# Performance work log

Hardware: AMD Instinct MI355X
Metric: run time of the kernel (lower is better)

The kernel has to match this reference:

```python
import jax, jax.numpy as jnp
import numpy as np

NEG_INF = -9e15
ALPHA = 0.2  # leaky_relu slope


def gat_layer(h, adj, e_feat, W, We, a_s, a_d, a_e, h_res):
    """Dense multi-head GAT layer with edge features.
    h: [B,N,Fin], adj: [B,N,N] (0/1), e_feat: [B,N,N,Ein]
    W: [H,Fin,Fout], We: [H,Ein,Eout], a_s/a_d: [H,Fout], a_e: [H,Eout]
    Returns head-averaged (x_prime [B,N,Fout], e_prime [B,N,N,Eout]).
    """
    Wh = jnp.einsum('bnf,hfo->bhno', h, W)            # [B,H,N,Fout]
    Me = jnp.einsum('bnmf,hfe->bhnme', e_feat, We)    # [B,H,N,N,Eout]
    s_src = jnp.einsum('bhno,ho->bhn', Wh, a_s)
    s_dst = jnp.einsum('bhno,ho->bhn', Wh, a_d)
    s_edge = jnp.einsum('bhnme,he->bhnm', Me, a_e)
    scores = jax.nn.leaky_relu(s_src[:, :, :, None] + s_dst[:, :, None, :] + s_edge, ALPHA)
    scores = jnp.where(adj[:, None, :, :] > 0, scores, NEG_INF)
    att = jax.nn.softmax(scores, axis=-1)             # [B,H,N,N]
    h_prime = jnp.einsum('bhnm,bhmo->bhno', att, Wh)
    h_prime = jax.nn.elu(h_prime) + h_res[:, None]    # concat=True -> elu; residual add
    e_prime = att[..., None] * Me                      # attention-modulated edge features
    return h_prime.mean(axis=1), e_prime.mean(axis=1)


def setup_inputs() -> dict:
    key = jax.random.key(0)
    ks = jax.random.split(key, 16)
    B, N, F, E, H = 2, 256, 768, 7, 2
    nhid, ehid = 768, 768 // 2
    sc = lambda fan: 1.0 / np.sqrt(fan)
    return {
        'x': jax.random.normal(ks[0], (B, N, F), jnp.float32),
        'adj': jax.random.randint(ks[1], (B, N, N), 0, 2, jnp.int32),
        'e': jax.random.uniform(ks[2], (B, N, N, E), jnp.float32),
        'W1': jax.random.normal(ks[3], (H, F, nhid), jnp.float32) * sc(F),
        'We1': jax.random.normal(ks[4], (H, E, ehid), jnp.float32) * sc(E),
        'a1s': jax.random.normal(ks[5], (H, nhid), jnp.float32) * sc(nhid),
        'a1d': jax.random.normal(ks[6], (H, nhid), jnp.float32) * sc(nhid),
        'a1e': jax.random.normal(ks[7], (H, ehid), jnp.float32) * sc(ehid),
        'W2': jax.random.normal(ks[8], (H, nhid, nhid), jnp.float32) * sc(nhid),
        'We2': jax.random.normal(ks[9], (H, ehid, ehid), jnp.float32) * sc(ehid),
        'a2s': jax.random.normal(ks[10], (H, nhid), jnp.float32) * sc(nhid),
        'a2d': jax.random.normal(ks[11], (H, nhid), jnp.float32) * sc(nhid),
        'a2e': jax.random.normal(ks[12], (H, ehid), jnp.float32) * sc(ehid),
    }


def reference(x, adj, e, W1, We1, a1s, a1d, a1e, W2, We2, a2s, a2d, a2e):
    # dropout layers are identity in eval mode
    x1, e1 = gat_layer(x, adj, e, W1, We1, a1s, a1d, a1e, x)
    x2, e2 = gat_layer(x1, adj, e1, W2, We2, a2s, a2d, a2e, x)
    return x2, e2
```

## Files before the change

### kernel.cpp

```cpp
#include <hip/hip_runtime.h>
#include <hip/hip_bf16.h>
#include <cstddef>


typedef __attribute__((ext_vector_type(8))) short bf16x8;
typedef __attribute__((ext_vector_type(4))) short bf16x4;
typedef __attribute__((ext_vector_type(4))) float f32x4;
typedef unsigned short us;

#define DEVINL static __device__ __forceinline__

DEVINL us f2bf(float f) {
    union { float f; unsigned u; } v; v.f = f;
    return (us)((v.u + 0x7FFFu + ((v.u >> 16) & 1u)) >> 16);
}
DEVINL float bf2f(us b) {
    union { unsigned u; float f; } v; v.u = ((unsigned)b) << 16; return v.f;
}
DEVINL float wredmax(float v) {
#pragma unroll
    for (int s = 32; s; s >>= 1) v = fmaxf(v, __shfl_xor(v, s));
    return v;
}
DEVINL float wredsum(float v) {
#pragma unroll
    for (int s = 32; s; s >>= 1) v += __shfl_xor(v, s);
    return v;
}

DEVINL void transpose_body(const float* __restrict__ W, us* __restrict__ WT, int bb) {
    __shared__ us tile[64][65];
    const int ft = (bb % 12) * 64, ot = ((bb / 12) % 12) * 64, h = bb / 144;
    const int t = threadIdx.x;
    const float* Wh = W + (size_t)h * 768 * 768;
    us* WTh = WT + (size_t)h * 768 * 768;
#pragma unroll
    for (int i = 0; i < 16; i++) {
        int idx = t + i * 256, r = idx >> 6, c = idx & 63;
        tile[c][r] = f2bf(Wh[(ft + r) * 768 + ot + c]);
    }
    __syncthreads();
#pragma unroll
    for (int i = 0; i < 16; i++) {
        int idx = t + i * 256, r = idx >> 6, c = idx & 63;
        WTh[(ot + r) * 768 + ft + c] = tile[r][c];
    }
}

DEVINL void cvt_body(const float* __restrict__ in, us* __restrict__ out, int blk) {
    int i = (blk * 256 + threadIdx.x) * 4;
    float4 v = *(const float4*)&in[i];
    us pk[4] = {f2bf(v.x), f2bf(v.y), f2bf(v.z), f2bf(v.w)};
    *(bf16x4*)&out[i] = *(bf16x4*)pk;
}

DEVINL void pre_body(const float* __restrict__ W1, const float* __restrict__ W2,
                     const float* __restrict__ We1, const float* __restrict__ We2,
                     const float* __restrict__ a1s, const float* __restrict__ a1d,
                     const float* __restrict__ a1e, const float* __restrict__ a2s,
                     const float* __restrict__ a2d,
                     float* __restrict__ q, float* __restrict__ u1,
                     float* __restrict__ Mcat, int blk) {
    const int g = blk * 32 + (threadIdx.x >> 3);
    const int lane = threadIdx.x & 7;
    float acc = 0.0f;
    if (g < 6144) {
        int vec = g / 1536, rem = g % 1536, h = rem / 768, f = rem % 768;
        const float* W = (vec < 2) ? W1 : W2;
        const float* a = (vec == 0) ? a1s : (vec == 1) ? a1d : (vec == 2) ? a2s : a2d;
        const float* wr = W + (size_t)(h * 768 + f) * 768;
        const float* ar = a + h * 768;
        for (int o = lane; o < 768; o += 8) acc += wr[o] * ar[o];
        for (int s = 4; s; s >>= 1) acc += __shfl_down(acc, s, 8);
        if (lane == 0) q[g] = acc;
    } else if (g < 6160) {
        int g2 = g - 6144, h = g2 >> 3, k = g2 & 7;
        if (k < 7) {
            const float* wr = We1 + (h * 7 + k) * 384;
            const float* ar = a1e + h * 384;
            for (int o = lane; o < 384; o += 8) acc += wr[o] * ar[o];
        }
        for (int s = 4; s; s >>= 1) acc += __shfl_down(acc, s, 8);
        if (lane == 0) u1[g2] = acc;
    } else if (g < 18448) {
        int g3 = g - 6160, rk = g3 / 384, tc = g3 % 384;
        int hh = rk >> 3, kk = rk & 7, h1 = hh >> 1, h2 = hh & 1;
        if (kk < 7) {
            const float* wr = We1 + (h1 * 7 + kk) * 384;
            const float* w2c = We2 + (size_t)h2 * 384 * 384 + tc;
            for (int o = lane; o < 384; o += 8) acc += wr[o] * w2c[o * 384];
            acc *= 0.25f;
        }
        for (int s = 4; s; s >>= 1) acc += __shfl_down(acc, s, 8);
        if (lane == 0) Mcat[g3] = acc;
    }
}

DEVINL void wcalc_body(const float* __restrict__ Mcat, const float* __restrict__ a2e,
                       float* __restrict__ w) {
    const int t = threadIdx.x, g = t >> 3, lane = t & 7;
    int hh = g >> 3, k = g & 7, h2 = hh & 1;
    float acc = 0.0f;
    if (k < 7)
        for (int o = lane; o < 384; o += 8) acc += Mcat[(hh * 8 + k) * 384 + o] * a2e[h2 * 384 + o];
    for (int s = 4; s; s >>= 1) acc += __shfl_down(acc, s, 8);
    if (lane == 0) w[g] = 2.0f * acc;
}

DEVINL void bfrag_body(const float* __restrict__ Mcat, us* __restrict__ Bfrag, int ct) {
    const int l = threadIdx.x;
    if (l < 64) {
        us pk[8];
#pragma unroll
        for (int j = 0; j < 8; j++)
            pk[j] = f2bf(Mcat[((l >> 4) * 8 + j) * 384 + ct * 16 + (l & 15)]);
        *(bf16x8*)&Bfrag[(ct * 64 + l) * 8] = *(bf16x8*)pk;
    }
}

DEVINL void sdots_body(const float* __restrict__ x, const float* __restrict__ qs,
                       const float* __restrict__ qd, float* __restrict__ out_s,
                       float* __restrict__ out_d, int n, int b) {
    const int t = threadIdx.x, wv = t >> 6;
    const float* xr = x + (size_t)(b * 256 + n) * 768;
    float a0 = 0, a1 = 0, a2 = 0, a3 = 0;
#pragma unroll
    for (int i = 0; i < 3; i++) {
        int k = i * 256 + t;
        float xv = xr[k];
        a0 += xv * qs[k];
        a1 += xv * qs[768 + k];
        a2 += xv * qd[k];
        a3 += xv * qd[768 + k];
    }
    a0 = wredsum(a0); a1 = wredsum(a1); a2 = wredsum(a2); a3 = wredsum(a3);
    __shared__ float part[4][4];
    if ((t & 63) == 0) { part[wv][0] = a0; part[wv][1] = a1; part[wv][2] = a2; part[wv][3] = a3; }
    __syncthreads();
    if (t == 0) {
        float r0 = 0, r1 = 0, r2 = 0, r3 = 0;
#pragma unroll
        for (int i = 0; i < 4; i++) { r0 += part[i][0]; r1 += part[i][1]; r2 += part[i][2]; r3 += part[i][3]; }
        out_s[(b * 2 + 0) * 256 + n] = r0;
        out_s[(b * 2 + 1) * 256 + n] = r1;
        out_d[(b * 2 + 0) * 256 + n] = r2;
        out_d[(b * 2 + 1) * 256 + n] = r3;
    }
}

DEVINL void att_finish(float sc, us* __restrict__ attb, size_t outbase) {
    const int m = threadIdx.x, wv = m >> 6;
    __shared__ float sm[4], ssu[4];
    float wm_ = wredmax(sc);
    if ((m & 63) == 0) sm[wv] = wm_;
    __syncthreads();
    float mx = fmaxf(fmaxf(sm[0], sm[1]), fmaxf(sm[2], sm[3]));
    float ex = __expf(sc - mx);
    float ws = wredsum(ex);
    if ((m & 63) == 0) ssu[wv] = ws;
    __syncthreads();
    float inv = 1.0f / (ssu[0] + ssu[1] + ssu[2] + ssu[3]);
    attb[outbase + m] = f2bf(ex * inv);
}

DEVINL void att1_body(const float* __restrict__ e, const int* __restrict__ adj,
                      const float* __restrict__ s_s, const float* __restrict__ s_d,
                      const float* __restrict__ u1, us* __restrict__ attb,
                      int n, int h, int b) {
    const int m = threadIdx.x;
    float ss = s_s[(b * 2 + h) * 256 + n];
    float sd = s_d[(b * 2 + h) * 256 + m];
    const float* ep = e + ((size_t)(b * 256 + n) * 256 + m) * 7;
    float se = 0.0f;
#pragma unroll
    for (int k = 0; k < 7; k++) se += ep[k] * u1[h * 8 + k];
    float sc = ss + sd + se;
    sc = sc > 0.0f ? sc : 0.2f * sc;
    sc = adj[(size_t)(b * 256 + n) * 256 + m] > 0 ? sc : -9e15f;
    att_finish(sc, attb, ((size_t)(b * 2 + h) * 256 + n) * 256);
}

DEVINL void att2_body(const float* __restrict__ e, const int* __restrict__ adj,
                      const float* __restrict__ s_s, const float* __restrict__ s_d,
                      const float* __restrict__ w, const us* __restrict__ att1b,
                      us* __restrict__ attb, int n, int h, int b) {
    const int m = threadIdx.x;
    float ss = s_s[(b * 2 + h) * 256 + n];
    float sd = s_d[(b * 2 + h) * 256 + m];
    const float* ep = e + ((size_t)(b * 256 + n) * 256 + m) * 7;
    float se = 0.0f;
#pragma unroll
    for (int h1 = 0; h1 < 2; h1++) {
        float ew = 0.0f;
#pragma unroll
        for (int k = 0; k < 7; k++) ew += ep[k] * w[(h1 * 2 + h) * 8 + k];
        float a1 = bf2f(att1b[((size_t)(b * 2 + h1) * 256 + n) * 256 + m]);
        se += a1 * ew;
    }
    float sc = ss + sd + se;
    sc = sc > 0.0f ? sc : 0.2f * sc;
    sc = adj[(size_t)(b * 256 + n) * 256 + m] > 0 ? sc : -9e15f;
    att_finish(sc, attb, ((size_t)(b * 2 + h) * 256 + n) * 256);
}

DEVINL void gemm_xw_body(const us* __restrict__ A, const us* __restrict__ BT,
                         us* __restrict__ WhT, int mt, int ot, int h) {
    const int t = threadIdx.x, wv = t >> 6, l = t & 63;
    const int wm = wv >> 1, wn = wv & 1, lr = l & 15, lk = l >> 4;
    __shared__ us As[64][40];
    __shared__ us Bs[64][40];
    const int arow = t >> 2, acol = (t & 3) * 8;
    const us* Bh = BT + (size_t)h * 768 * 768;
    f32x4 acc[2][2];
#pragma unroll
    for (int i = 0; i < 2; i++)
#pragma unroll
        for (int j = 0; j < 2; j++) acc[i][j] = (f32x4){0, 0, 0, 0};
    for (int k0 = 0; k0 < 768; k0 += 32) {
        __syncthreads();
        *(bf16x8*)&As[arow][acol] = *(const bf16x8*)&A[(size_t)(mt * 64 + arow) * 768 + k0 + acol];
        *(bf16x8*)&Bs[arow][acol] = *(const bf16x8*)&Bh[(size_t)(ot * 64 + arow) * 768 + k0 + acol];
        __syncthreads();
        bf16x8 af[2], bfv[2];
#pragma unroll
        for (int i = 0; i < 2; i++) af[i] = *(const bf16x8*)&As[wm * 32 + i * 16 + lr][lk * 8];
#pragma unroll
        for (int j = 0; j < 2; j++) bfv[j] = *(const bf16x8*)&Bs[wn * 32 + j * 16 + lr][lk * 8];
#pragma unroll
        for (int i = 0; i < 2; i++)
#pragma unroll
            for (int j = 0; j < 2; j++)
                acc[i][j] = __builtin_amdgcn_mfma_f32_16x16x32_bf16(af[i], bfv[j], acc[i][j], 0, 0, 0);
    }
#pragma unroll
    for (int i = 0; i < 2; i++)
#pragma unroll
        for (int j = 0; j < 2; j++) {
            int n0 = mt * 64 + wm * 32 + i * 16 + lk * 4;
            int og = ot * 64 + wn * 32 + j * 16 + lr;
            int b = n0 >> 8, n = n0 & 255;
            us pk[4];
#pragma unroll
            for (int r = 0; r < 4; r++) pk[r] = f2bf(acc[i][j][r]);
            *(bf16x4*)&WhT[((size_t)(b * 2 + h) * 768 + og) * 256 + n] = *(bf16x4*)pk;
        }
}

DEVINL void gemm_att_body(const us* __restrict__ attb, const us* __restrict__ WhT,
                          const float* __restrict__ resid, float* __restrict__ xout,
                          us* __restrict__ xbout, int mt, int ot, int b) {
    const int t = threadIdx.x, wv = t >> 6, l = t & 63;
    const int wm = wv >> 1, wn = wv & 1, lr = l & 15, lk = l >> 4;
    __shared__ us As2[64][40];
    __shared__ us Bs2[64][40];
    const int arow = t >> 2, acol = (t & 3) * 8;
    float res[2][2][4] = {};
    for (int h = 0; h < 2; h++) {
        const us* Ah = attb + (size_t)(b * 2 + h) * 256 * 256;
        const us* Bh = WhT + (size_t)(b * 2 + h) * 768 * 256;
        f32x4 acc[2][2];
#pragma unroll
        for (int i = 0; i < 2; i++)
#pragma unroll
            for (int j = 0; j < 2; j++) acc[i][j] = (f32x4){0, 0, 0, 0};
        for (int k0 = 0; k0 < 256; k0 += 32) {
            __syncthreads();
            *(bf16x8*)&As2[arow][acol] = *(const bf16x8*)&Ah[(size_t)(mt * 64 + arow) * 256 + k0 + acol];
            *(bf16x8*)&Bs2[arow][acol] = *(const bf16x8*)&Bh[(size_t)(ot * 64 + arow) * 256 + k0 + acol];
            __syncthreads();
            bf16x8 af[2], bfv[2];
#pragma unroll
            for (int i = 0; i < 2; i++) af[i] = *(const bf16x8*)&As2[wm * 32 + i * 16 + lr][lk * 8];
#pragma unroll
            for (int j = 0; j < 2; j++) bfv[j] = *(const bf16x8*)&Bs2[wn * 32 + j * 16 + lr][lk * 8];
#pragma unroll
            for (int i = 0; i < 2; i++)
#pragma unroll
                for (int j = 0; j < 2; j++)
                    acc[i][j] = __builtin_amdgcn_mfma_f32_16x16x32_bf16(af[i], bfv[j], acc[i][j], 0, 0, 0);
        }
#pragma unroll
        for (int i = 0; i < 2; i++)
#pragma unroll
            for (int j = 0; j < 2; j++)
#pragma unroll
                for (int r = 0; r < 4; r++) {
                    float v = acc[i][j][r];
                    res[i][j][r] += (v > 0.0f ? v : (expf(v) - 1.0f));
                }
        __syncthreads();
    }
#pragma unroll
    for (int i = 0; i < 2; i++)
#pragma unroll
        for (int j = 0; j < 2; j++) {
            int n0 = mt * 64 + wm * 32 + i * 16 + lk * 4;
            int og = ot * 64 + wn * 32 + j * 16 + lr;
#pragma unroll
            for (int r = 0; r < 4; r++) {
                size_t idx = (size_t)(b * 256 + n0 + r) * 768 + og;
                float v = 0.5f * res[i][j][r] + resid[idx];
                xout[idx] = v;
                if (xbout) xbout[idx] = f2bf(v);
            }
        }
}

DEVINL void e2_body(const float* __restrict__ e, const us* __restrict__ att1b,
                    const us* __restrict__ att2b, const us* __restrict__ Bfrag,
                    float* __restrict__ e2out, int eb, int cg) {
    __shared__ us bl[8 * 64 * 8];
    const int t = threadIdx.x;
    for (int idx = t; idx < 512; idx += 256)
        *(bf16x8*)&bl[idx * 8] = *(const bf16x8*)&Bfrag[(size_t)(cg * 512 + idx) * 8];
    __syncthreads();
    const int wv = t >> 6, l = t & 63, le = l & 15, lq = l >> 4;
    const int h1 = lq >> 1, h2 = lq & 1;
    bf16x8 bfr[8];
#pragma unroll
    for (int i = 0; i < 8; i++) bfr[i] = *(const bf16x8*)&bl[(i * 64 + l) * 8];
    const f32x4 zero = {0, 0, 0, 0};
    for (int g = 0; g < 4; g++) {
        const int ebase = eb * 256 + g * 64 + wv * 16;
        const int eidx = ebase + le;
        const int b = eidx >> 16, nm = eidx & 65535;
        float a1 = bf2f(att1b[(size_t)(b * 2 + h1) * 65536 + nm]);
        float a2 = bf2f(att2b[(size_t)(b * 2 + h2) * 65536 + nm]);
        float c = a1 * a2;
        const float* ep = e + (size_t)eidx * 7;
        us av[8];
#pragma unroll
        for (int j = 0; j < 7; j++) av[j] = f2bf(c * ep[j]);
        av[7] = 0;
        bf16x8 gfr = *(bf16x8*)av;
#pragma unroll
        for (int i = 0; i < 8; i++) {
            f32x4 accv = __builtin_amdgcn_mfma_f32_16x16x32_bf16(bfr[i], gfr, zero, 0, 0, 0);
            int o0 = cg * 128 + i * 16 + lq * 4;
            *(f32x4*)&e2out[(size_t)eidx * 384 + o0] = accv;
        }
    }
}

__global__ __launch_bounds__(256) void stage1(
    const float* W1, const float* W2, const float* We1, const float* We2,
    const float* a1s, const float* a1d, const float* a1e,
    const float* a2s, const float* a2d,
    const float* x, us* W1T, us* W2T, us* xb,
    float* q, float* u1, float* Mcat) {
    int b = blockIdx.x;
    if (b < 288)       transpose_body(W1, W1T, b);
    else if (b < 576)  transpose_body(W2, W2T, b - 288);
    else if (b < 960)  cvt_body(x, xb, b - 576);
    else               pre_body(W1, W2, We1, We2, a1s, a1d, a1e, a2s, a2d, q, u1, Mcat, b - 960);
}

__global__ __launch_bounds__(256) void stage2(
    const float* Mcat, const float* a2e, float* wbuf, us* Bfrag,
    const float* x, const float* qs, const float* qd, float* s1s, float* s1d) {
    int b = blockIdx.x;
    if (b < 1)        wcalc_body(Mcat, a2e, wbuf);
    else if (b < 25)  bfrag_body(Mcat, Bfrag, b - 1);
    else { int i = b - 25; sdots_body(x, qs, qd, s1s, s1d, i & 255, i >> 8); }
}

__global__ __launch_bounds__(256) void stage3(
    const float* e, const int* adj, const float* s1s, const float* s1d,
    const float* u1, us* att1b, const us* xb, const us* W1T, us* WhT1) {
    int b = blockIdx.x;
    if (b < 1024) att1_body(e, adj, s1s, s1d, u1, att1b, b & 255, (b >> 8) & 1, b >> 9);
    else { int g = b - 1024; gemm_xw_body(xb, W1T, WhT1, g & 7, (g >> 3) % 12, g / 96); }
}

__global__ __launch_bounds__(256) void stage4(
    const us* att1b, const us* WhT1, const float* x, float* x1, us* xb1) {
    int b = blockIdx.x;
    gemm_att_body(att1b, WhT1, x, x1, xb1, b & 3, (b >> 2) % 12, b / 48);
}

__global__ __launch_bounds__(256) void stage5(
    const float* x1, const float* qs, const float* qd, float* s2s, float* s2d,
    const us* xb1, const us* W2T, us* WhT2) {
    int b = blockIdx.x;
    if (b < 512) sdots_body(x1, qs, qd, s2s, s2d, b & 255, b >> 8);
    else { int g = b - 512; gemm_xw_body(xb1, W2T, WhT2, g & 7, (g >> 3) % 12, g / 96); }
}

__global__ __launch_bounds__(256) void stage6(
    const float* e, const int* adj, const float* s2s, const float* s2d,
    const float* wbuf, const us* att1b, us* att2b) {
    int b = blockIdx.x;
    att2_body(e, adj, s2s, s2d, wbuf, att1b, att2b, b & 255, (b >> 8) & 1, b >> 9);
}

__global__ __launch_bounds__(256) void stage7(
    const us* att2b, const us* WhT2, const float* x, float* x2out,
    const float* e, const us* att1b, const us* Bfrag, float* e2out) {
    int b = blockIdx.x;
    if (b < 96) gemm_att_body(att2b, WhT2, x, x2out, (us*)nullptr, b & 3, (b >> 2) % 12, b / 48);
    else { int idx = b - 96; e2_body(e, att1b, att2b, Bfrag, e2out, idx / 3, idx % 3); }
}

__global__ __launch_bounds__(256) void stage8(
    const float* e, const us* att1b, const us* att2b, const us* Bfrag, float* e2out) {
    int b = blockIdx.x;
    e2_body(e, att1b, att2b, Bfrag, e2out, 508 + b / 3, b % 3);
}

extern "C" void kernel_launch(void* const* d_in, const int* in_sizes, int n_in,
                              void* d_out, int out_size, void* d_ws, size_t ws_size,
                              hipStream_t stream) {
    const float* x   = (const float*)d_in[0];
    const int*   adj = (const int*)d_in[1];
    const float* e   = (const float*)d_in[2];
    const float* W1  = (const float*)d_in[3];
    const float* We1 = (const float*)d_in[4];
    const float* a1s = (const float*)d_in[5];
    const float* a1d = (const float*)d_in[6];
    const float* a1e = (const float*)d_in[7];
    const float* W2  = (const float*)d_in[8];
    const float* We2 = (const float*)d_in[9];
    const float* a2s = (const float*)d_in[10];
    const float* a2d = (const float*)d_in[11];
    const float* a2e = (const float*)d_in[12];

    float* out   = (float*)d_out;
    float* x2out = out;
    float* e2out = out + 393216;

    char* ws = (char*)d_ws;
    float* q     = (float*)(ws + 0);
    float* u1    = (float*)(ws + 24576);
    float* wbuf  = (float*)(ws + 24640);
    float* Mcat  = (float*)(ws + 24832);
    us*    Bfrag = (us*)(ws + 73984);
    float* s1s   = (float*)(ws + 98560);
    float* s1d   = (float*)(ws + 102656);
    float* s2s   = (float*)(ws + 106752);
    float* s2d   = (float*)(ws + 110848);
    us*    att1b = (us*)(ws + 114944);
    us*    att2b = (us*)(ws + 639232);

    char* sc = (char*)e2out;
    us*    W1T  = (us*)(sc + 0);
    us*    W2T  = (us*)(sc + 2359296);
    us*    xb   = (us*)(sc + 4718592);
    us*    xb1  = (us*)(sc + 5505024);
    us*    WhT1 = (us*)(sc + 6291456);
    float* x1   = (float*)(sc + 7864320);
    us*    WhT2 = (us*)(e2out + 49938432);

    stage1<<<1537, 256, 0, stream>>>(W1, W2, We1, We2, a1s, a1d, a1e, a2s, a2d,
                                     x, W1T, W2T, xb, q, u1, Mcat);
    stage2<<<537, 256, 0, stream>>>(Mcat, a2e, wbuf, Bfrag, x, q + 0, q + 1536, s1s, s1d);
    stage3<<<1216, 256, 0, stream>>>(e, adj, s1s, s1d, u1, att1b, xb, W1T, WhT1);
    stage4<<<96, 256, 0, stream>>>(att1b, WhT1, x, x1, xb1);
    stage5<<<704, 256, 0, stream>>>(x1, q + 3072, q + 4608, s2s, s2d, xb1, W2T, WhT2);
    stage6<<<1024, 256, 0, stream>>>(e, adj, s2s, s2d, wbuf, att1b, att2b);
    stage7<<<1620, 256, 0, stream>>>(att2b, WhT2, x, x2out, e, att1b, Bfrag, e2out);
    stage8<<<12, 256, 0, stream>>>(e, att1b, att2b, Bfrag, e2out);
}
```

Baseline: 118.3 us.

## Fuse both heads per attention row, retile att GEMM, row-wise e2, move scratch to workspace

Attention-score kernels now process both heads per block, staging the edge-feature row in shared memory once instead of reading it per head. The att@Wh GEMM is retiled to 32-row tiles to double block count, and the e2 output kernel now handles one full (b,n) row per block with all three column groups, removing the tail stage8 launch. Transpose and convert bodies use wider vector stores, scratch buffers move from the output region into the workspace, and stage1 block order is reshuffled. Larger shared-memory use in e2row may reduce occupancy.

```diff
diff --git a/kernel.cpp b/kernel.cpp
--- a/kernel.cpp
+++ b/kernel.cpp
@@ -41,17 +41,22 @@
     }
     __syncthreads();
 #pragma unroll
-    for (int i = 0; i < 16; i++) {
-        int idx = t + i * 256, r = idx >> 6, c = idx & 63;
-        WTh[(ot + r) * 768 + ft + c] = tile[r][c];
+    for (int i = 0; i < 2; i++) {
+        int idx = t + i * 256, r = idx >> 3, c0 = (idx & 7) * 8;
+        us pk[8];
+#pragma unroll
+        for (int j = 0; j < 8; j++) pk[j] = tile[r][c0 + j];
+        *(bf16x8*)&WTh[(ot + r) * 768 + ft + c0] = *(bf16x8*)pk;
     }
 }
 
 DEVINL void cvt_body(const float* __restrict__ in, us* __restrict__ out, int blk) {
-    int i = (blk * 256 + threadIdx.x) * 4;
-    float4 v = *(const float4*)&in[i];
-    us pk[4] = {f2bf(v.x), f2bf(v.y), f2bf(v.z), f2bf(v.w)};
-    *(bf16x4*)&out[i] = *(bf16x4*)pk;
+    int i = (blk * 256 + threadIdx.x) * 8;
+    float4 v0 = *(const float4*)&in[i];
+    float4 v1 = *(const float4*)&in[i + 4];
+    us pk[8] = {f2bf(v0.x), f2bf(v0.y), f2bf(v0.z), f2bf(v0.w),
+                f2bf(v1.x), f2bf(v1.y), f2bf(v1.z), f2bf(v1.w)};
+    *(bf16x8*)&out[i] = *(bf16x8*)pk;
 }
 
 DEVINL void pre_body(const float* __restrict__ W1, const float* __restrict__ W2,
@@ -148,59 +153,88 @@
     }
 }
 
-DEVINL void att_finish(float sc, us* __restrict__ attb, size_t outbase) {
-    const int m = threadIdx.x, wv = m >> 6;
-    __shared__ float sm[4], ssu[4];
-    float wm_ = wredmax(sc);
-    if ((m & 63) == 0) sm[wv] = wm_;
-    __syncthreads();
-    float mx = fmaxf(fmaxf(sm[0], sm[1]), fmaxf(sm[2], sm[3]));
-    float ex = __expf(sc - mx);
-    float ws = wredsum(ex);
-    if ((m & 63) == 0) ssu[wv] = ws;
-    __syncthreads();
-    float inv = 1.0f / (ssu[0] + ssu[1] + ssu[2] + ssu[3]);
-    attb[outbase + m] = f2bf(ex * inv);
+DEVINL void att_finish2(float sc0, float sc1, us* __restrict__ attb,
+                        size_t base0, size_t base1) {
+    const int t = threadIdx.x, wv = t >> 6;
+    __shared__ float smax[2][4], ssum[2][4];
+    float w0 = wredmax(sc0), w1 = wredmax(sc1);
+    if ((t & 63) == 0) { smax[0][wv] = w0; smax[1][wv] = w1; }
+    __syncthreads();
+    float mx0 = fmaxf(fmaxf(smax[0][0], smax[0][1]), fmaxf(smax[0][2], smax[0][3]));
+    float mx1 = fmaxf(fmaxf(smax[1][0], smax[1][1]), fmaxf(smax[1][2], smax[1][3]));
+    float ex0 = __expf(sc0 - mx0), ex1 = __expf(sc1 - mx1);
+    float su0 = wredsum(ex0), su1 = wredsum(ex1);
+    if ((t & 63) == 0) { ssum[0][wv] = su0; ssum[1][wv] = su1; }
+    __syncthreads();
+    float i0 = 1.0f / (ssum[0][0] + ssum[0][1] + ssum[0][2] + ssum[0][3]);
+    float i1 = 1.0f / (ssum[1][0] + ssum[1][1] + ssum[1][2] + ssum[1][3]);
+    attb[base0 + t] = f2bf(ex0 * i0);
+    attb[base1 + t] = f2bf(ex1 * i1);
 }
 
 DEVINL void att1_body(const float* __restrict__ e, const int* __restrict__ adj,
                       const float* __restrict__ s_s, const float* __restrict__ s_d,
                       const float* __restrict__ u1, us* __restrict__ attb,
-                      int n, int h, int b) {
-    const int m = threadIdx.x;
-    float ss = s_s[(b * 2 + h) * 256 + n];
-    float sd = s_d[(b * 2 + h) * 256 + m];
-    const float* ep = e + ((size_t)(b * 256 + n) * 256 + m) * 7;
-    float se = 0.0f;
-#pragma unroll
-    for (int k = 0; k < 7; k++) se += ep[k] * u1[h * 8 + k];
-    float sc = ss + sd + se;
-    sc = sc > 0.0f ? sc : 0.2f * sc;
-    sc = adj[(size_t)(b * 256 + n) * 256 + m] > 0 ? sc : -9e15f;
-    att_finish(sc, attb, ((size_t)(b * 2 + h) * 256 + n) * 256);
+                      int n, int bb) {
+    __shared__ float eL[1792];
+    const int t = threadIdx.x;
+    const float* erow = e + (size_t)(bb * 256 + n) * 256 * 7;
+#pragma unroll
+    for (int i = 0; i < 7; i++) eL[t + i * 256] = erow[t + i * 256];
+    __syncthreads();
+    float ss0 = s_s[(bb * 2 + 0) * 256 + n], ss1 = s_s[(bb * 2 + 1) * 256 + n];
+    float sd0 = s_d[(bb * 2 + 0) * 256 + t], sd1 = s_d[(bb * 2 + 1) * 256 + t];
+    float se0 = 0, se1 = 0;
+#pragma unroll
+    for (int k = 0; k < 7; k++) {
+        float ev = eL[t * 7 + k];
+        se0 += ev * u1[k];
+        se1 += ev * u1[8 + k];
+    }
+    float sc0 = ss0 + sd0 + se0, sc1 = ss1 + sd1 + se1;
+    sc0 = sc0 > 0.0f ? sc0 : 0.2f * sc0;
+    sc1 = sc1 > 0.0f ? sc1 : 0.2f * sc1;
+    bool ok = adj[(size_t)(bb * 256 + n) * 256 + t] > 0;
+    sc0 = ok ? sc0 : -9e15f;
+    sc1 = ok ? sc1 : -9e15f;
+    size_t base0 = ((size_t)(bb * 2 + 0) * 256 + n) * 256;
+    size_t base1 = ((size_t)(bb * 2 + 1) * 256 + n) * 256;
+    att_finish2(sc0, sc1, attb, base0, base1);
 }
 
 DEVINL void att2_body(const float* __restrict__ e, const int* __restrict__ adj,
                       const float* __restrict__ s_s, const float* __restrict__ s_d,
                       const float* __restrict__ w, const us* __restrict__ att1b,
-                      us* __restrict__ attb, int n, int h, int b) {
-    const int m = threadIdx.x;
-    float ss = s_s[(b * 2 + h) * 256 + n];
-    float sd = s_d[(b * 2 + h) * 256 + m];
-    const float* ep = e + ((size_t)(b * 256 + n) * 256 + m) * 7;
-    float se = 0.0f;
-#pragma unroll
-    for (int h1 = 0; h1 < 2; h1++) {
-        float ew = 0.0f;
-#pragma unroll
-        for (int k = 0; k < 7; k++) ew += ep[k] * w[(h1 * 2 + h) * 8 + k];
-        float a1 = bf2f(att1b[((size_t)(b * 2 + h1) * 256 + n) * 256 + m]);
-        se += a1 * ew;
-    }
-    float sc = ss + sd + se;
-    sc = sc > 0.0f ? sc : 0.2f * sc;
-    sc = adj[(size_t)(b * 256 + n) * 256 + m] > 0 ? sc : -9e15f;
-    att_finish(sc, attb, ((size_t)(b * 2 + h) * 256 + n) * 256);
+                      us* __restrict__ attb, int n, int bb) {
+    __shared__ float eL[1792];
+    const int t = threadIdx.x;
+    const float* erow = e + (size_t)(bb * 256 + n) * 256 * 7;
+#pragma unroll
+    for (int i = 0; i < 7; i++) eL[t + i * 256] = erow[t + i * 256];
+    __syncthreads();
+    float ss0 = s_s[(bb * 2 + 0) * 256 + n], ss1 = s_s[(bb * 2 + 1) * 256 + n];
+    float sd0 = s_d[(bb * 2 + 0) * 256 + t], sd1 = s_d[(bb * 2 + 1) * 256 + t];
+    float a10 = bf2f(att1b[((size_t)(bb * 2 + 0) * 256 + n) * 256 + t]);
+    float a11 = bf2f(att1b[((size_t)(bb * 2 + 1) * 256 + n) * 256 + t]);
+    float ew00 = 0, ew01 = 0, ew10 = 0, ew11 = 0;
+#pragma unroll
+    for (int k = 0; k < 7; k++) {
+        float ev = eL[t * 7 + k];
+        ew00 += ev * w[0 * 8 + k];
+        ew01 += ev * w[1 * 8 + k];
+        ew10 += ev * w[2 * 8 + k];
+        ew11 += ev * w[3 * 8 + k];
+    }
+    float sc0 = ss0 + sd0 + a10 * ew00 + a11 * ew10;
+    float sc1 = ss1 + sd1 + a10 * ew01 + a11 * ew11;
+    sc0 = sc0 > 0.0f ? sc0 : 0.2f * sc0;
+    sc1 = sc1 > 0.0f ? sc1 : 0.2f * sc1;
+    bool ok = adj[(size_t)(bb * 256 + n) * 256 + t] > 0;
+    sc0 = ok ? sc0 : -9e15f;
+    sc1 = ok ? sc1 : -9e15f;
+    size_t base0 = ((size_t)(bb * 2 + 0) * 256 + n) * 256;
+    size_t base1 = ((size_t)(bb * 2 + 1) * 256 + n) * 256;
+    att_finish2(sc0, sc1, attb, base0, base1);
 }
 
 DEVINL void gemm_xw_body(const us* __restrict__ A, const us* __restrict__ BT,
@@ -251,93 +285,101 @@
                           us* __restrict__ xbout, int mt, int ot, int b) {
     const int t = threadIdx.x, wv = t >> 6, l = t & 63;
     const int wm = wv >> 1, wn = wv & 1, lr = l & 15, lk = l >> 4;
-    __shared__ us As2[64][40];
+    __shared__ us As2[32][40];
     __shared__ us Bs2[64][40];
-    const int arow = t >> 2, acol = (t & 3) * 8;
-    float res[2][2][4] = {};
+    float res[2][4] = {};
     for (int h = 0; h < 2; h++) {
-        const us* Ah = attb + (size_t)(b * 2 + h) * 256 * 256;
+        const us* Ah = attb + (size_t)(b * 2 + h) * 65536;
         const us* Bh = WhT + (size_t)(b * 2 + h) * 768 * 256;
-        f32x4 acc[2][2];
-#pragma unroll
-        for (int i = 0; i < 2; i++)
-#pragma unroll
-            for (int j = 0; j < 2; j++) acc[i][j] = (f32x4){0, 0, 0, 0};
+        f32x4 acc[2];
+        acc[0] = (f32x4){0, 0, 0, 0};
+        acc[1] = (f32x4){0, 0, 0, 0};
         for (int k0 = 0; k0 < 256; k0 += 32) {
             __syncthreads();
-            *(bf16x8*)&As2[arow][acol] = *(const bf16x8*)&Ah[(size_t)(mt * 64 + arow) * 256 + k0 + acol];
-            *(bf16x8*)&Bs2[arow][acol] = *(const bf16x8*)&Bh[(size_t)(ot * 64 + arow) * 256 + k0 + acol];
+            if (t < 128) {
+                int ar = t >> 2, ac = (t & 3) * 8;
+                *(bf16x8*)&As2[ar][ac] = *(const bf16x8*)&Ah[(size_t)(mt * 32 + ar) * 256 + k0 + ac];
+            }
+            {
+                int br = t >> 2, bc = (t & 3) * 8;
+                *(bf16x8*)&Bs2[br][bc] = *(const bf16x8*)&Bh[(size_t)(ot * 64 + br) * 256 + k0 + bc];
+            }
             __syncthreads();
-            bf16x8 af[2], bfv[2];
-#pragma unroll
-            for (int i = 0; i < 2; i++) af[i] = *(const bf16x8*)&As2[wm * 32 + i * 16 + lr][lk * 8];
-#pragma unroll
-            for (int j = 0; j < 2; j++) bfv[j] = *(const bf16x8*)&Bs2[wn * 32 + j * 16 + lr][lk * 8];
-#pragma unroll
-            for (int i = 0; i < 2; i++)
-#pragma unroll
-                for (int j = 0; j < 2; j++)
-                    acc[i][j] = __builtin_amdgcn_mfma_f32_16x16x32_bf16(af[i], bfv[j], acc[i][j], 0, 0, 0);
-        }
-#pragma unroll
-        for (int i = 0; i < 2; i++)
-#pragma unroll
-            for (int j = 0; j < 2; j++)
-#pragma unroll
-                for (int r = 0; r < 4; r++) {
-                    float v = acc[i][j][r];
-                    res[i][j][r] += (v > 0.0f ? v : (expf(v) - 1.0f));
-                }
+            bf16x8 af = *(const bf16x8*)&As2[wm * 16 + lr][lk * 8];
+#pragma unroll
+            for (int j = 0; j < 2; j++) {
+                bf16x8 bv = *(const bf16x8*)&Bs2[wn * 32 + j * 16 + lr][lk * 8];
+                acc[j] = __builtin_amdgcn_mfma_f32_16x16x32_bf16(af, bv, acc[j], 0, 0, 0);
+            }
+        }
+#pragma unroll
+        for (int j = 0; j < 2; j++)
+#pragma unroll
+            for (int r = 0; r < 4; r++) {
+                float v = acc[j][r];
+                res[j][r] += (v > 0.0f ? v : (expf(v) - 1.0f));
+            }
         __syncthreads();
     }
 #pragma unroll
-    for (int i = 0; i < 2; i++)
-#pragma unroll
-        for (int j = 0; j < 2; j++) {
-            int n0 = mt * 64 + wm * 32 + i * 16 + lk * 4;
-            int og = ot * 64 + wn * 32 + j * 16 + lr;
-#pragma unroll
-            for (int r = 0; r < 4; r++) {
-                size_t idx = (size_t)(b * 256 + n0 + r) * 768 + og;
-                float v = 0.5f * res[i][j][r] + resid[idx];
-                xout[idx] = v;
-                if (xbout) xbout[idx] = f2bf(v);
-            }
-        }
-}
-
-DEVINL void e2_body(const float* __restrict__ e, const us* __restrict__ att1b,
-                    const us* __restrict__ att2b, const us* __restrict__ Bfrag,
-                    float* __restrict__ e2out, int eb, int cg) {
-    __shared__ us bl[8 * 64 * 8];
+    for (int j = 0; j < 2; j++) {
+        int n0 = mt * 32 + wm * 16 + lk * 4;
+        int og = ot * 64 + wn * 32 + j * 16 + lr;
+#pragma unroll
+        for (int r = 0; r < 4; r++) {
+            size_t idx = (size_t)(b * 256 + n0 + r) * 768 + og;
+            float v = 0.5f * res[j][r] + resid[idx];
+            xout[idx] = v;
+            if (xbout) xbout[idx] = f2bf(v);
+        }
+    }
+}
+
+DEVINL void e2row_body(const float* __restrict__ e, const us* __restrict__ att1b,
+                       const us* __restrict__ att2b, const us* __restrict__ Bfrag,
+                       float* __restrict__ e2out, int bb, int n) {
+    __shared__ us blB[1536 * 8];
+    __shared__ float eL[1792];
+    __shared__ float aL[4][256];
     const int t = threadIdx.x;
-    for (int idx = t; idx < 512; idx += 256)
-        *(bf16x8*)&bl[idx * 8] = *(const bf16x8*)&Bfrag[(size_t)(cg * 512 + idx) * 8];
+    for (int i = t; i < 1536; i += 256)
+        *(bf16x8*)&blB[i * 8] = *(const bf16x8*)&Bfrag[(size_t)i * 8];
+    const float* erow = e + (size_t)(bb * 256 + n) * 256 * 7;
+#pragma unroll
+    for (int i = 0; i < 7; i++) eL[t + i * 256] = erow[t + i * 256];
+    const size_t abase = (size_t)bb * 2 * 65536 + n * 256;
+    aL[0][t] = bf2f(att1b[abase + t]);
+    aL[1][t] = bf2f(att1b[abase + 65536 + t]);
+    aL[2][t] = bf2f(att2b[abase + t]);
+    aL[3][t] = bf2f(att2b[abase + 65536 + t]);
     __syncthreads();
     const int wv = t >> 6, l = t & 63, le = l & 15, lq = l >> 4;
     const int h1 = lq >> 1, h2 = lq & 1;
-    bf16x8 bfr[8];
-#pragma unroll
-    for (int i = 0; i < 8; i++) bfr[i] = *(const bf16x8*)&bl[(i * 64 + l) * 8];
+    bf16x8 av[4];
+#pragma unroll
+    for (int g = 0; g < 4; g++) {
+        int m = g * 64 + wv * 16 + le;
+        float c = aL[h1][m] * aL[2 + h2][m];
+        us pk[8];
+#pragma unroll
+        for (int j = 0; j < 7; j++) pk[j] = f2bf(c * eL[m * 7 + j]);
+        pk[7] = 0;
+        av[g] = *(bf16x8*)pk;
+    }
     const f32x4 zero = {0, 0, 0, 0};
-    for (int g = 0; g < 4; g++) {
-        const int ebase = eb * 256 + g * 64 + wv * 16;
-        const int eidx = ebase + le;
-        const int b = eidx >> 16, nm = eidx & 65535;
-        float a1 = bf2f(att1b[(size_t)(b * 2 + h1) * 65536 + nm]);
-        float a2 = bf2f(att2b[(size_t)(b * 2 + h2) * 65536 + nm]);
-        float c = a1 * a2;
-        const float* ep = e + (size_t)eidx * 7;
-        us av[8];
-#pragma unroll
-        for (int j = 0; j < 7; j++) av[j] = f2bf(c * ep[j]);
-        av[7] = 0;
-        bf16x8 gfr = *(bf16x8*)av;
-#pragma unroll
-        for (int i = 0; i < 8; i++) {
-            f32x4 accv = __builtin_amdgcn_mfma_f32_16x16x32_bf16(bfr[i], gfr, zero, 0, 0, 0);
-            int o0 = cg * 128 + i * 16 + lq * 4;
-            *(f32x4*)&e2out[(size_t)eidx * 384 + o0] = accv;
+    const size_t rowbase = (size_t)bb * 65536 + n * 256;
+#pragma unroll
+    for (int cg = 0; cg < 3; cg++) {
+        bf16x8 bfr[8];
+#pragma unroll
+        for (int i = 0; i < 8; i++) bfr[i] = *(const bf16x8*)&blB[(cg * 512 + i * 64 + l) * 8];
+        for (int g = 0; g < 4; g++) {
+            size_t eidx = rowbase + g * 64 + wv * 16 + le;
+#pragma unroll
+            for (int i = 0; i < 8; i++) {
+                f32x4 acc = __builtin_amdgcn_mfma_f32_16x16x32_bf16(bfr[i], av[g], zero, 0, 0, 0);
+                *(f32x4*)&e2out[eidx * 384 + cg * 128 + i * 16 + lq * 4] = acc;
+            }
         }
     }
 }
@@ -349,10 +391,10 @@
     const float* x, us* W1T, us* W2T, us* xb,
     float* q, float* u1, float* Mcat) {
     int b = blockIdx.x;
-    if (b < 288)       transpose_body(W1, W1T, b);
-    else if (b < 576)  transpose_body(W2, W2T, b - 288);
-    else if (b < 960)  cvt_body(x, xb, b - 576);
-    else               pre_body(W1, W2, We1, We2, a1s, a1d, a1e, a2s, a2d, q, u1, Mcat, b - 960);
+    if (b < 577)       pre_body(W1, W2, We1, We2, a1s, a1d, a1e, a2s, a2d, q, u1, Mcat, b);
+    else if (b < 865)  transpose_body(W1, W1T, b - 577);
+    else if (b < 1153) transpose_body(W2, W2T, b - 865);
+    else               cvt_body(x, xb, b - 1153);
 }
 
 __global__ __launch_bounds__(256) void stage2(
@@ -368,14 +410,14 @@
     const float* e, const int* adj, const float* s1s, const float* s1d,
     const float* u1, us* att1b, const us* xb, const us* W1T, us* WhT1) {
     int b = blockIdx.x;
-    if (b < 1024) att1_body(e, adj, s1s, s1d, u1, att1b, b & 255, (b >> 8) & 1, b >> 9);
-    else { int g = b - 1024; gemm_xw_body(xb, W1T, WhT1, g & 7, (g >> 3) % 12, g / 96); }
+    if (b < 512) att1_body(e, adj, s1s, s1d, u1, att1b, b & 255, b >> 8);
+    else { int g = b - 512; gemm_xw_body(xb, W1T, WhT1, g & 7, (g >> 3) % 12, g / 96); }
 }
 
 __global__ __launch_bounds__(256) void stage4(
     const us* att1b, const us* WhT1, const float* x, float* x1, us* xb1) {
     int b = blockIdx.x;
-    gemm_att_body(att1b, WhT1, x, x1, xb1, b & 3, (b >> 2) % 12, b / 48);
+    gemm_att_body(att1b, WhT1, x, x1, xb1, b & 7, (b >> 3) % 12, b / 96);
 }
 
 __global__ __launch_bounds__(256) void stage5(
@@ -390,21 +432,15 @@
     const float* e, const int* adj, const float* s2s, const float* s2d,
     const float* wbuf, const us* att1b, us* att2b) {
     int b = blockIdx.x;
-    att2_body(e, adj, s2s, s2d, wbuf, att1b, att2b, b & 255, (b >> 8) & 1, b >> 9);
+    att2_body(e, adj, s2s, s2d, wbuf, att1b, att2b, b & 255, b >> 8);
 }
 
 __global__ __launch_bounds__(256) void stage7(
     const us* att2b, const us* WhT2, const float* x, float* x2out,
     const float* e, const us* att1b, const us* Bfrag, float* e2out) {
     int b = blockIdx.x;
-    if (b < 96) gemm_att_body(att2b, WhT2, x, x2out, (us*)nullptr, b & 3, (b >> 2) % 12, b / 48);
-    else { int idx = b - 96; e2_body(e, att1b, att2b, Bfrag, e2out, idx / 3, idx % 3); }
-}
-
-__global__ __launch_bounds__(256) void stage8(
-    const float* e, const us* att1b, const us* att2b, const us* Bfrag, float* e2out) {
-    int b = blockIdx.x;
-    e2_body(e, att1b, att2b, Bfrag, e2out, 508 + b / 3, b % 3);
+    if (b < 192) gemm_att_body(att2b, WhT2, x, x2out, (us*)nullptr, b & 7, (b >> 3) % 12, b / 96);
+    else { int r = b - 192; e2row_body(e, att1b, att2b, Bfrag, e2out, r >> 8, r & 255); }
 }
 
 extern "C" void kernel_launch(void* const* d_in, const int* in_sizes, int n_in,
@@ -440,23 +476,20 @@
     float* s2d   = (float*)(ws + 110848);
     us*    att1b = (us*)(ws + 114944);
     us*    att2b = (us*)(ws + 639232);
-
-    char* sc = (char*)e2out;
-    us*    W1T  = (us*)(sc + 0);
-    us*    W2T  = (us*)(sc + 2359296);
-    us*    xb   = (us*)(sc + 4718592);
-    us*    xb1  = (us*)(sc + 5505024);
-    us*    WhT1 = (us*)(sc + 6291456);
-    float* x1   = (float*)(sc + 7864320);
-    us*    WhT2 = (us*)(e2out + 49938432);
-
-    stage1<<<1537, 256, 0, stream>>>(W1, W2, We1, We2, a1s, a1d, a1e, a2s, a2d,
+    us*    W1T   = (us*)(ws + 1163520);
+    us*    W2T   = (us*)(ws + 3522816);
+    us*    xb    = (us*)(ws + 5882112);
+    us*    xb1   = (us*)(ws + 6668544);
+    us*    WhT1  = (us*)(ws + 7454976);
+    us*    WhT2  = (us*)(ws + 9027840);
+    float* x1    = (float*)(ws + 10600704);
+
+    stage1<<<1345, 256, 0, stream>>>(W1, W2, We1, We2, a1s, a1d, a1e, a2s, a2d,
                                      x, W1T, W2T, xb, q, u1, Mcat);
     stage2<<<537, 256, 0, stream>>>(Mcat, a2e, wbuf, Bfrag, x, q + 0, q + 1536, s1s, s1d);
-    stage3<<<1216, 256, 0, stream>>>(e, adj, s1s, s1d, u1, att1b, xb, W1T, WhT1);
-    stage4<<<96, 256, 0, stream>>>(att1b, WhT1, x, x1, xb1);
+    stage3<<<704, 256, 0, stream>>>(e, adj, s1s, s1d, u1, att1b, xb, W1T, WhT1);
+    stage4<<<192, 256, 0, stream>>>(att1b, WhT1, x, x1, xb1);
     stage5<<<704, 256, 0, stream>>>(x1, q + 3072, q + 4608, s2s, s2d, xb1, W2T, WhT2);
-    stage6<<<1024, 256, 0, stream>>>(e, adj, s2s, s2d, wbuf, att1b, att2b);
-    stage7<<<1620, 256, 0, stream>>>(att2b, WhT2, x, x2out, e, att1b, Bfrag, e2out);
-    stage8<<<12, 256, 0, stream>>>(e, att1b, att2b, Bfrag, e2out);
-}
+    stage6<<<512, 256, 0, stream>>>(e, adj, s2s, s2d, wbuf, att1b, att2b);
+    stage7<<<704, 256, 0, stream>>>(att2b, WhT2, x, x2out, e, att1b, Bfrag, e2out);
+}
```

Measured after the change: 106.0 us. -10.4%, faster.
